# Optimization experiments

Hardware: AMD Instinct MI355X
Metric: run time of the kernel (lower is better)

Reference implementation:

```python
import jax, jax.numpy as jnp
import numpy as np

HIDDEN = 512
HEADS = 8
HEAD_DIM = HIDDEN // HEADS
THRESH = 0.1
EPS = 1e-8


def setup_inputs() -> dict:
    key = jax.random.key(0)
    ks = jax.random.split(key, 9)
    B, S = 2, 4096
    scale = 1.0 / np.sqrt(HIDDEN)
    x = jax.random.normal(ks[0], (B, S, HIDDEN), dtype=jnp.float32)
    Wq = jax.random.normal(ks[1], (HIDDEN, HIDDEN), dtype=jnp.float32) * scale
    bq = jnp.zeros((HIDDEN,), dtype=jnp.float32)
    Wk = jax.random.normal(ks[2], (HIDDEN, HIDDEN), dtype=jnp.float32) * scale
    bk = jnp.zeros((HIDDEN,), dtype=jnp.float32)
    Wv = jax.random.normal(ks[3], (HIDDEN, HIDDEN), dtype=jnp.float32) * scale
    bv = jnp.zeros((HIDDEN,), dtype=jnp.float32)
    Wo = jax.random.normal(ks[4], (HIDDEN, HIDDEN), dtype=jnp.float32) * scale
    bo = jnp.zeros((HIDDEN,), dtype=jnp.float32)
    return {"x": x, "Wq": Wq, "bq": bq, "Wk": Wk, "bk": bk,
            "Wv": Wv, "bv": bv, "Wo": Wo, "bo": bo}


def reference(x, Wq, bq, Wk, bk, Wv, bv, Wo, bo):
    B, S, _ = x.shape
    # torch Linear: y = x @ W.T + b
    def proj(W, b):
        y = jnp.einsum('bsd,ed->bse', x, W) + b
        return y.reshape(B, S, HEADS, HEAD_DIM).transpose(0, 2, 1, 3)  # [B,H,S,Dh]
    Q = proj(Wq, bq)
    K = proj(Wk, bk)
    V = proj(Wv, bv)
    scores = jnp.einsum('bhqd,bhkd->bhqk', Q, K) / jnp.sqrt(jnp.float32(HEAD_DIM))
    probs = jax.nn.softmax(scores, axis=-1)  # [B,H,S,S]
    probs = jnp.where(probs > THRESH, probs, 0.0)
    probs = probs / (jnp.sum(probs, axis=-1, keepdims=True) + EPS)
    ctx = jnp.einsum('bhqk,bhkd->bhqd', probs, V)
    ctx = ctx.transpose(0, 2, 1, 3).reshape(B, S, HIDDEN)
    return jnp.einsum('bsd,ed->bse', ctx, Wo) + bo
```

## Files before the change

kernel.cpp:

```cpp
#include <hip/hip_runtime.h>

#define S_LEN 4096
#define BATCH 2
#define HID 512
#define HEADS 8
#define HD 64
#define NX (BATCH * S_LEN * HID)
#define WSZ (HID * HID)
#define NBH (BATCH * HEADS)
#define QB 64
#define NBLK (S_LEN / QB * NBH)

typedef short v8s __attribute__((ext_vector_type(8)));
typedef float v4f __attribute__((ext_vector_type(4)));
typedef float v16f __attribute__((ext_vector_type(16)));
typedef unsigned short ushort_t;
typedef const __attribute__((address_space(1))) unsigned gu32;
typedef __attribute__((address_space(3))) unsigned lu32;

__device__ __forceinline__ ushort_t f2bf(float f) {
  unsigned u = __builtin_bit_cast(unsigned, f);
  u += 0x7fffu + ((u >> 16) & 1u);
  return (ushort_t)(u >> 16);
}
__device__ __forceinline__ unsigned pk2(float a, float b) {
  return (__builtin_bit_cast(unsigned, a) >> 16) |
         (__builtin_bit_cast(unsigned, b) & 0xFFFF0000u);
}
__device__ __forceinline__ float fexp2(float x) {
  return __builtin_amdgcn_exp2f(x);
}


__global__ __launch_bounds__(256) void cvt_k(
    const float* __restrict__ x,
    const float* __restrict__ wq, const float* __restrict__ wk,
    const float* __restrict__ wv, const float* __restrict__ wo,
    ushort_t* __restrict__ dst)
{
  const size_t e = ((size_t)blockIdx.x * 256 + threadIdx.x) * 4;
  const float* src; size_t off;
  if (e < NX) { src = x; off = e; }
  else {
    const size_t we = e - NX;
    const int wi = (int)(we >> 18);
    src = wi == 0 ? wq : wi == 1 ? wk : wi == 2 ? wv : wo;
    off = we & (WSZ - 1);
  }
  float4 v = *(const float4*)&src[off];
  uint2 u; u.x = pk2(v.x, v.y); u.y = pk2(v.z, v.w);
  *(uint2*)&dst[e] = u;
}

__global__ __launch_bounds__(256) void gemm_qkv(
    const ushort_t* __restrict__ X, const ushort_t* __restrict__ Wb,
    const float* __restrict__ bq, const float* __restrict__ bk, const float* __restrict__ bv,
    ushort_t* __restrict__ Qf, ushort_t* __restrict__ Kf, ushort_t* __restrict__ Vw,
    float qscale)
{
  __shared__ ushort_t As[128][32];
  __shared__ ushort_t Bs[128][32];
  const int t = threadIdx.x;
  const int lane = t & 63;
  const int l15 = lane & 15, lg = lane >> 4;
  const int w = t >> 6;
  const int wr = w >> 1, wc = w & 1;
  const int m0 = blockIdx.y * 128;
  const int wsel = blockIdx.x >> 2;
  const int e0 = (blockIdx.x & 3) * 128;
  const ushort_t* W = Wb + (size_t)wsel * WSZ;
  const float* bias = wsel == 0 ? bq : wsel == 1 ? bk : bv;
  const float osc = (wsel == 0) ? qscale : 1.0f;

  v4f acc[4][4] = {};
  const int r0  = t >> 2;
  const int c0  = (t & 3) * 8;
  const int sc0 = (((t & 3) ^ ((t >> 3) & 3))) * 8;
  const int rsw = (l15 >> 1) & 3;

  for (int k0 = 0; k0 < HID; k0 += 32) {
    __syncthreads();
    __builtin_amdgcn_global_load_lds(
        (gu32*)(const void*)&X[(size_t)(m0 + r0) * HID + k0 + sc0],
        (lu32*)(void*)&As[r0][c0], 16, 0, 0);
    __builtin_amdgcn_global_load_lds(
        (gu32*)(const void*)&X[(size_t)(m0 + r0 + 64) * HID + k0 + sc0],
        (lu32*)(void*)&As[r0 + 64][c0], 16, 0, 0);
    __builtin_amdgcn_global_load_lds(
        (gu32*)(const void*)&W[(size_t)(e0 + r0) * HID + k0 + sc0],
        (lu32*)(void*)&Bs[r0][c0], 16, 0, 0);
    __builtin_amdgcn_global_load_lds(
        (gu32*)(const void*)&W[(size_t)(e0 + r0 + 64) * HID + k0 + sc0],
        (lu32*)(void*)&Bs[r0 + 64][c0], 16, 0, 0);
    __syncthreads();
    v8s a[4], b[4];
    #pragma unroll
    for (int fr = 0; fr < 4; ++fr)
      a[fr] = *(const v8s*)&As[wr * 64 + 16 * fr + l15][8 * (lg ^ rsw)];
    #pragma unroll
    for (int fc = 0; fc < 4; ++fc)
      b[fc] = *(const v8s*)&Bs[wc * 64 + 16 * fc + l15][8 * (lg ^ rsw)];
    #pragma unroll
    for (int fr = 0; fr < 4; ++fr)
      #pragma unroll
      for (int fc = 0; fc < 4; ++fc)
        acc[fr][fc] = __builtin_amdgcn_mfma_f32_16x16x32_bf16(a[fr], b[fc], acc[fr][fc], 0, 0, 0);
  }

  #pragma unroll
  for (int fr = 0; fr < 4; ++fr)
    #pragma unroll
    for (int fc = 0; fc < 4; ++fc) {
      const int e = e0 + wc * 64 + 16 * fc + l15;
      const float bval = bias[e];
      #pragma unroll
      for (int r = 0; r < 4; ++r) {
        const int m = m0 + wr * 64 + 16 * fr + 4 * lg + r;
        const float v = (acc[fr][fc][r] + bval) * osc;
        const int bidx = m >> 12, s = m & (S_LEN - 1);
        const int hh = e >> 6, dh = e & 63;
        const size_t hb = ((size_t)(bidx * HEADS + hh)) * (size_t)(S_LEN * HD);
        if (wsel == 2) {
          Vw[hb + (size_t)s * HD + dh] = f2bf(v);
        } else {
          const size_t off = (size_t)(s >> 5) * 2048 +
              (size_t)(((dh >> 4) * 64 + ((dh >> 3) & 1) * 32 + (s & 31)) * 8 + (dh & 7));
          (wsel == 0 ? Qf : Kf)[hb + off] = f2bf(v);
        }
      }
    }
}

__global__ __launch_bounds__(512, 4) void attn_p1(
    const ushort_t* __restrict__ Qf, const ushort_t* __restrict__ Kf,
    int* __restrict__ Flg)
{
  __shared__ float RedL[4][QB];
  __shared__ float RedM[4][QB];
  __shared__ int bflag;
  const int t = threadIdx.x;
  const int lane = t & 63;
  const int l31 = lane & 31, hi = lane >> 5;
  const int w = t >> 6;
  const int rs = w >> 2;
  const int kq = w & 3;
  const int lin = blockIdx.x;
  const int bh = ((lin & 7) << 1) | ((lin >> 3) & 1);
  const int q0 = (lin >> 4) * QB;
  if (t == 0) bflag = 0;

  const size_t hoff = (size_t)bh * (size_t)(S_LEN * HD);
  const ushort_t* Qb = Qf + hoff + ((size_t)(q0 >> 5) + rs) * 2048;
  const ushort_t* Kb = Kf + hoff;

  v8s qa[4];
  #pragma unroll
  for (int ks = 0; ks < 4; ++ks)
    qa[ks] = *(const v8s*)&Qb[(ks * 64 + lane) * 8];

  float M[16], L[16];
  #pragma unroll
  for (int j = 0; j < 16; ++j) { M[j] = -1e30f; L[j] = 0.f; }

  v8s kA[4], kB[4];

#define LOADK(DST, IDX)                                                     \
  {                                                                         \
    const ushort_t* kc_ = Kb + (size_t)(kq + 4 * (IDX)) * 2048;             \
    _Pragma("unroll")                                                       \
    for (int ks = 0; ks < 4; ++ks)                                          \
      DST[ks] = *(const v8s*)&kc_[(ks * 64 + lane) * 8];                    \
  }
#define CHAIN(KX, OUT)                                                      \
  {                                                                         \
    v16f s_ = {};                                                           \
    _Pragma("unroll")                                                       \
    for (int ks = 0; ks < 4; ++ks)                                          \
      s_ = __builtin_amdgcn_mfma_f32_32x32x16_bf16(qa[ks], KX[ks], s_, 0, 0, 0); \
    OUT = s_;                                                               \
  }
#define MERGE(P)                                                            \
  {                                                                         \
    _Pragma("unroll")                                                       \
    for (int j = 0; j < 16; ++j) {                                          \
      M[j] = fmaxf(M[j], P[j]);                                             \
      L[j] += fexp2(P[j]);                                                  \
    }                                                                       \
  }

  LOADK(kA, 0)
  LOADK(kB, 1)
  v16f prev, cur;
  CHAIN(kA, prev)
  for (int i = 1; i < 31; i += 2) {
    LOADK(kA, i + 1)
    CHAIN(kB, cur)
    MERGE(prev)
    prev = cur;
    LOADK(kB, i + 2)
    CHAIN(kA, cur)
    MERGE(prev)
    prev = cur;
  }
  CHAIN(kB, cur)
  MERGE(prev)
  MERGE(cur)
#undef LOADK
#undef CHAIN
#undef MERGE

  #pragma unroll
  for (int j = 0; j < 16; ++j) {
    float Lv = L[j], Mv = M[j];
    Lv += __shfl_xor(Lv, 1);  Mv = fmaxf(Mv, __shfl_xor(Mv, 1));
    Lv += __shfl_xor(Lv, 2);  Mv = fmaxf(Mv, __shfl_xor(Mv, 2));
    Lv += __shfl_xor(Lv, 4);  Mv = fmaxf(Mv, __shfl_xor(Mv, 4));
    Lv += __shfl_xor(Lv, 8);  Mv = fmaxf(Mv, __shfl_xor(Mv, 8));
    Lv += __shfl_xor(Lv, 16); Mv = fmaxf(Mv, __shfl_xor(Mv, 16));
    if (l31 == 0) {
      const int row = rs * 32 + (j & 3) + 8 * (j >> 2) + 4 * hi;
      RedL[kq][row] = Lv;
      RedM[kq][row] = Mv;
    }
  }
  __syncthreads();
  if (t < QB) {
    const float Lv = RedL[0][t] + RedL[1][t] + RedL[2][t] + RedL[3][t];
    const float Mv = fmaxf(fmaxf(RedM[0][t], RedM[1][t]),
                           fmaxf(RedM[2][t], RedM[3][t]));
    if (Mv >= __log2f(Lv) - 3.3719281f) atomicOr(&bflag, 1);
  }
  __syncthreads();
  if (t == 0) Flg[lin] = bflag;
}

__global__ __launch_bounds__(256) void attn_p2(
    const ushort_t* __restrict__ Qf, const ushort_t* __restrict__ Kf,
    const ushort_t* __restrict__ V, ushort_t* __restrict__ Cb,
    const int* __restrict__ Flg)
{
  const int lin = blockIdx.x;
  if (Flg[lin] == 0) return;
  __shared__ float Osh[QB][HD + 1];
  __shared__ float Dsh[QB];
  __shared__ float RedA[4][QB];
  __shared__ float iLs[QB];
  __shared__ ushort_t Pp[4][32][40];
  __shared__ ushort_t VT[4][HD][40];
  const int t = threadIdx.x;
  const int lane = t & 63;
  const int l31 = lane & 31, hi = lane >> 5;
  const int w = t >> 6;
  const int bh = ((lin & 7) << 1) | ((lin >> 3) & 1);
  const int q0 = (lin >> 4) * QB;
  const size_t hoff = (size_t)bh * (size_t)(S_LEN * HD);
  const ushort_t* Qb = Qf + hoff + (size_t)(q0 >> 5) * 2048;
  const ushort_t* Kb = Kf + hoff;
  const ushort_t* Vh = V + hoff;

  if (t < QB) Dsh[t] = 0.f;
  for (int idx = t; idx < QB * HD; idx += 256) Osh[idx >> 6][idx & 63] = 0.f;

  v8s qa[4], qB[4];
  #pragma unroll
  for (int ks = 0; ks < 4; ++ks) {
    qa[ks] = *(const v8s*)&Qb[(ks * 64 + lane) * 8];
    qB[ks] = *(const v8s*)&Qb[2048 + (ks * 64 + lane) * 8];
  }

  float L0[16], L1[16];
  #pragma unroll
  for (int j = 0; j < 16; ++j) { L0[j] = 0.f; L1[j] = 0.f; }
  for (int i = 0; i < 32; ++i) {
    const ushort_t* kc = Kb + (size_t)(w + 4 * i) * 2048;
    v8s kb[4];
    #pragma unroll
    for (int ks = 0; ks < 4; ++ks)
      kb[ks] = *(const v8s*)&kc[(ks * 64 + lane) * 8];
    v16f sa = {}, sb = {};
    #pragma unroll
    for (int ks = 0; ks < 4; ++ks) {
      sa = __builtin_amdgcn_mfma_f32_32x32x16_bf16(qa[ks], kb[ks], sa, 0, 0, 0);
      sb = __builtin_amdgcn_mfma_f32_32x32x16_bf16(qB[ks], kb[ks], sb, 0, 0, 0);
    }
    #pragma unroll
    for (int j = 0; j < 16; ++j) {
      L0[j] += fexp2(sa[j]);
      L1[j] += fexp2(sb[j]);
    }
  }
  #pragma unroll
  for (int rseti = 0; rseti < 2; ++rseti)
    #pragma unroll
    for (int j = 0; j < 16; ++j) {
      float Lv = (rseti == 0) ? L0[j] : L1[j];
      Lv += __shfl_xor(Lv, 1);  Lv += __shfl_xor(Lv, 2);
      Lv += __shfl_xor(Lv, 4);  Lv += __shfl_xor(Lv, 8);
      Lv += __shfl_xor(Lv, 16);
      if (l31 == 0) {
        const int row = rseti * 32 + (j & 3) + 8 * (j >> 2) + 4 * hi;
        RedA[w][row] = Lv;
      }
    }
  __syncthreads();
  if (t < QB)
    iLs[t] = 1.0f / (RedA[0][t] + RedA[1][t] + RedA[2][t] + RedA[3][t]);
  __syncthreads();

  float il[2][16];
  #pragma unroll
  for (int rseti = 0; rseti < 2; ++rseti)
    #pragma unroll
    for (int j = 0; j < 16; ++j)
      il[rseti][j] = iLs[rseti * 32 + (j & 3) + 8 * (j >> 2) + 4 * hi];

  v16f oA[2] = {}, oB[2] = {};
  float den[2][16] = {};

  for (int i = 0; i < 32; ++i) {
    const int c = w + 4 * i;
    const ushort_t* kc = Kb + (size_t)c * 2048;
    v8s kb[4];
    #pragma unroll
    for (int ks = 0; ks < 4; ++ks)
      kb[ks] = *(const v8s*)&kc[(ks * 64 + lane) * 8];
    v16f sa = {}, sb = {};
    #pragma unroll
    for (int ks = 0; ks < 4; ++ks) {
      sa = __builtin_amdgcn_mfma_f32_32x32x16_bf16(qa[ks], kb[ks], sa, 0, 0, 0);
      sb = __builtin_amdgcn_mfma_f32_32x32x16_bf16(qB[ks], kb[ks], sb, 0, 0, 0);
    }
    {
      const ushort_t* vsrc = &Vh[((size_t)c * 32 + l31) * HD + hi * 32];
      #pragma unroll
      for (int qq = 0; qq < 4; ++qq) {
        uint4 vv = *(const uint4*)&vsrc[qq * 8];
        const ushort_t* pv = (const ushort_t*)&vv;
        #pragma unroll
        for (int jj = 0; jj < 8; ++jj)
          VT[w][hi * 32 + qq * 8 + jj][l31] = pv[jj];
      }
    }
    #pragma unroll
    for (int rseti = 0; rseti < 2; ++rseti) {
      #pragma unroll
      for (int j = 0; j < 16; ++j) {
        const float s = (rseti == 0) ? sa[j] : sb[j];
        const int row = (j & 3) + 8 * (j >> 2) + 4 * hi;
        float p = fexp2(s) * il[rseti][j];
        p = (p > 0.1f) ? p : 0.f;
        den[rseti][j] += p;
        Pp[w][row][l31] = f2bf(p);
      }
      v8s pa0 = *(const v8s*)&Pp[w][l31][8 * hi];
      v8s pa1 = *(const v8s*)&Pp[w][l31][16 + 8 * hi];
      #pragma unroll
      for (int dblk = 0; dblk < 2; ++dblk) {
        v8s vb0 = *(const v8s*)&VT[w][dblk * 32 + l31][8 * hi];
        v8s vb1 = *(const v8s*)&VT[w][dblk * 32 + l31][16 + 8 * hi];
        if (rseti == 0) {
          oA[dblk] = __builtin_amdgcn_mfma_f32_32x32x16_bf16(pa0, vb0, oA[dblk], 0, 0, 0);
          oA[dblk] = __builtin_amdgcn_mfma_f32_32x32x16_bf16(pa1, vb1, oA[dblk], 0, 0, 0);
        } else {
          oB[dblk] = __builtin_amdgcn_mfma_f32_32x32x16_bf16(pa0, vb0, oB[dblk], 0, 0, 0);
          oB[dblk] = __builtin_amdgcn_mfma_f32_32x32x16_bf16(pa1, vb1, oB[dblk], 0, 0, 0);
        }
      }
    }
  }

  #pragma unroll
  for (int rseti = 0; rseti < 2; ++rseti)
    #pragma unroll
    for (int j = 0; j < 16; ++j) {
      float d = den[rseti][j];
      d += __shfl_xor(d, 1); d += __shfl_xor(d, 2); d += __shfl_xor(d, 4);
      d += __shfl_xor(d, 8); d += __shfl_xor(d, 16);
      const int row = rseti * 32 + (j & 3) + 8 * (j >> 2) + 4 * hi;
      if (l31 == 0) atomicAdd(&Dsh[row], d);
    }
  #pragma unroll
  for (int rseti = 0; rseti < 2; ++rseti)
    #pragma unroll
    for (int dblk = 0; dblk < 2; ++dblk)
      #pragma unroll
      for (int j = 0; j < 16; ++j) {
        const int row = rseti * 32 + (j & 3) + 8 * (j >> 2) + 4 * hi;
        const float val = (rseti == 0) ? oA[dblk][j] : oB[dblk][j];
        atomicAdd(&Osh[row][dblk * 32 + l31], val);
      }
  __syncthreads();
  const int b = bh >> 3, h = bh & 7;
  for (int idx = t; idx < QB * HD; idx += 256) {
    const int row = idx >> 6, d = idx & 63;
    const float val = Osh[row][d] / (Dsh[row] + 1e-8f);
    Cb[((size_t)b * S_LEN + q0 + row) * HID + h * HD + d] = f2bf(val);
  }
}

__global__ __launch_bounds__(256) void gemm_out(
    const ushort_t* __restrict__ X, const ushort_t* __restrict__ W,
    const float* __restrict__ bias, const int* __restrict__ Flg,
    float* __restrict__ Df)
{
  const int t = threadIdx.x;
  const int m0 = blockIdx.y * 64;
  const int e0 = blockIdx.x * 64;

  int fm = 0;
  {
    const int b = m0 >> 12, qblk = (m0 & (S_LEN - 1)) >> 6;
    #pragma unroll
    for (int h = 0; h < HEADS; ++h) {
      const int bhh = b * HEADS + h;
      const int base = (bhh >> 1) | ((bhh & 1) << 3);
      fm |= (Flg[base | (qblk << 4)] ? 1 : 0) << h;
    }
    if (!fm) {
      const int row = t >> 2, c0 = (t & 3) * 16;
      #pragma unroll
      for (int g = 0; g < 4; ++g) {
        const float4 bv = *(const float4*)&bias[e0 + c0 + g * 4];
        *(float4*)&Df[(size_t)(m0 + row) * HID + e0 + c0 + g * 4] = bv;
      }
      return;
    }
  }

  __shared__ ushort_t As[64][40];
  __shared__ ushort_t Bs[64][40];
  const int lane = t & 63;
  const int l15 = lane & 15, lg = lane >> 4;
  const int w = t >> 6;
  const int wr = w >> 1, wc = w & 1;

  v4f acc[2][2] = {};
  const int srow = t >> 2, scol = (t & 3) * 8;
  const uint4 zu = {0u, 0u, 0u, 0u};

  for (int k0 = 0; k0 < HID; k0 += 32) {
    __syncthreads();
    const bool hot = (fm >> (k0 >> 6)) & 1;
    *(uint4*)&As[srow][scol] = hot
        ? *(const uint4*)&X[(size_t)(m0 + srow) * HID + k0 + scol]
        : zu;
    *(uint4*)&Bs[srow][scol] =
        *(const uint4*)&W[(size_t)(e0 + srow) * HID + k0 + scol];
    __syncthreads();
    v8s a[2], b[2];
    #pragma unroll
    for (int fr = 0; fr < 2; ++fr)
      a[fr] = *(const v8s*)&As[wr * 32 + 16 * fr + l15][8 * lg];
    #pragma unroll
    for (int fc = 0; fc < 2; ++fc)
      b[fc] = *(const v8s*)&Bs[wc * 32 + 16 * fc + l15][8 * lg];
    #pragma unroll
    for (int fr = 0; fr < 2; ++fr)
      #pragma unroll
      for (int fc = 0; fc < 2; ++fc)
        acc[fr][fc] = __builtin_amdgcn_mfma_f32_16x16x32_bf16(a[fr], b[fc], acc[fr][fc], 0, 0, 0);
  }

  #pragma unroll
  for (int fr = 0; fr < 2; ++fr)
    #pragma unroll
    for (int fc = 0; fc < 2; ++fc) {
      const int e = e0 + wc * 32 + 16 * fc + l15;
      const float bval = bias[e];
      #pragma unroll
      for (int r = 0; r < 4; ++r) {
        const int m = m0 + wr * 32 + 16 * fr + 4 * lg + r;
        Df[(size_t)m * HID + e] = acc[fr][fc][r] + bval;
      }
    }
}

extern "C" void kernel_launch(void* const* d_in, const int* in_sizes, int n_in,
                              void* d_out, int out_size, void* d_ws, size_t ws_size,
                              hipStream_t stream) {
  const float* x  = (const float*)d_in[0];
  const float* Wq = (const float*)d_in[1];
  const float* bq = (const float*)d_in[2];
  const float* Wk = (const float*)d_in[3];
  const float* bk = (const float*)d_in[4];
  const float* Wv = (const float*)d_in[5];
  const float* bv = (const float*)d_in[6];
  const float* Wo = (const float*)d_in[7];
  const float* bo = (const float*)d_in[8];

  int*      Flg  = (int*)d_ws;
  ushort_t* xb   = (ushort_t*)(Flg + NBLK);
  ushort_t* wqb  = xb + NX;
  ushort_t* wob  = wqb + 3 * WSZ;
  ushort_t* Qf   = wob + WSZ;
  ushort_t* Kf   = Qf + NX;
  ushort_t* Vw   = Kf + NX;
  ushort_t* Cb   = Vw + NX;

  const float qscale = 0.125f * 1.44269504f;

  cvt_k<<<(NX + 4 * WSZ) / 1024, 256, 0, stream>>>(x, Wq, Wk, Wv, Wo, xb);

  gemm_qkv<<<dim3(12, 64), 256, 0, stream>>>(
      xb, wqb, bq, bk, bv, Qf, Kf, Vw, qscale);

  attn_p1<<<NBLK, 512, 0, stream>>>(Qf, Kf, Flg);
  attn_p2<<<NBLK, 256, 0, stream>>>(Qf, Kf, Vw, Cb, Flg);

  gemm_out<<<dim3(8, 128), 256, 0, stream>>>(Cb, wob, bo, Flg, (float*)d_out);
}
```

Measured before the change: 103.5 us.

## Switch attention pass-1 scoring to 16x16x32 MFMA with new Q/K fragment layout

Changes the pre-packed Q/K layout from 32-row blocks sized for the 32x32x16 MFMA to 16-row blocks sized for the 16x16x32 bf16 MFMA. Pass 1 (row-max and sum screening) now computes scores as 2x2 tiles of 16x16 products, with smaller accumulators and a shorter shuffle reduction. Pass 2 still uses the 32x32 MFMA, so it now gathers its Q/K fragments element by element through the new layout. Those scalar 2-byte gathers replace the previous 16-byte vector loads and may cost more in pass 2 than pass 1 gains.

```diff
diff --git a/kernel.cpp b/kernel.cpp
--- a/kernel.cpp
+++ b/kernel.cpp
@@ -31,6 +31,10 @@
   return __builtin_amdgcn_exp2f(x);
 }
 
+__device__ __forceinline__ size_t off16(int s, int d) {
+  return (size_t)(s >> 4) * 1024 +
+         (size_t)((d >> 5) * 512 + (((s & 15) + 16 * ((d >> 3) & 3)) * 8) + (d & 7));
+}
 
 __global__ __launch_bounds__(256) void cvt_k(
     const float* __restrict__ x,
@@ -123,9 +127,7 @@
         if (wsel == 2) {
           Vw[hb + (size_t)s * HD + dh] = f2bf(v);
         } else {
-          const size_t off = (size_t)(s >> 5) * 2048 +
-              (size_t)(((dh >> 4) * 64 + ((dh >> 3) & 1) * 32 + (s & 31)) * 8 + (dh & 7));
-          (wsel == 0 ? Qf : Kf)[hb + off] = f2bf(v);
+          (wsel == 0 ? Qf : Kf)[hb + off16(s, dh)] = f2bf(v);
         }
       }
     }
@@ -140,7 +142,7 @@
   __shared__ int bflag;
   const int t = threadIdx.x;
   const int lane = t & 63;
-  const int l31 = lane & 31, hi = lane >> 5;
+  const int l15 = lane & 15, lg = (lane >> 4) & 3;
   const int w = t >> 6;
   const int rs = w >> 2;
   const int kq = w & 3;
@@ -150,57 +152,79 @@
   if (t == 0) bflag = 0;
 
   const size_t hoff = (size_t)bh * (size_t)(S_LEN * HD);
-  const ushort_t* Qb = Qf + hoff + ((size_t)(q0 >> 5) + rs) * 2048;
+  const ushort_t* Qb = Qf + hoff;
   const ushort_t* Kb = Kf + hoff;
 
-  v8s qa[4];
-  #pragma unroll
-  for (int ks = 0; ks < 4; ++ks)
-    qa[ks] = *(const v8s*)&Qb[(ks * 64 + lane) * 8];
-
-  float M[16], L[16];
-  #pragma unroll
-  for (int j = 0; j < 16; ++j) { M[j] = -1e30f; L[j] = 0.f; }
-
-  v8s kA[4], kB[4];
+  v8s qa[2][2];
+  const int qc0 = (q0 >> 4) + rs * 2;
+  #pragma unroll
+  for (int tq = 0; tq < 2; ++tq)
+    #pragma unroll
+    for (int ds = 0; ds < 2; ++ds)
+      qa[tq][ds] = *(const v8s*)&Qb[(size_t)(qc0 + tq) * 1024 + ds * 512 + lane * 8];
+
+  float M[2][4], L[2][4];
+  #pragma unroll
+  for (int tq = 0; tq < 2; ++tq)
+    #pragma unroll
+    for (int r = 0; r < 4; ++r) { M[tq][r] = -1e30f; L[tq][r] = 0.f; }
+
+  v8s kA[2][2], kB[2][2];
 
 #define LOADK(DST, IDX)                                                     \
   {                                                                         \
-    const ushort_t* kc_ = Kb + (size_t)(kq + 4 * (IDX)) * 2048;             \
+    const int kc_ = (kq + 4 * (IDX)) * 2;                                   \
     _Pragma("unroll")                                                       \
-    for (int ks = 0; ks < 4; ++ks)                                          \
-      DST[ks] = *(const v8s*)&kc_[(ks * 64 + lane) * 8];                    \
+    for (int tk = 0; tk < 2; ++tk)                                          \
+      _Pragma("unroll")                                                     \
+      for (int ds = 0; ds < 2; ++ds)                                        \
+        DST[tk][ds] = *(const v8s*)&Kb[(size_t)(kc_ + tk) * 1024 + ds * 512 + lane * 8]; \
   }
 #define CHAIN(KX, OUT)                                                      \
   {                                                                         \
-    v16f s_ = {};                                                           \
     _Pragma("unroll")                                                       \
-    for (int ks = 0; ks < 4; ++ks)                                          \
-      s_ = __builtin_amdgcn_mfma_f32_32x32x16_bf16(qa[ks], KX[ks], s_, 0, 0, 0); \
-    OUT = s_;                                                               \
+    for (int tq = 0; tq < 2; ++tq)                                          \
+      _Pragma("unroll")                                                     \
+      for (int tk = 0; tk < 2; ++tk) {                                      \
+        v4f s_ = {0.f, 0.f, 0.f, 0.f};                                      \
+        s_ = __builtin_amdgcn_mfma_f32_16x16x32_bf16(qa[tq][0], KX[tk][0], s_, 0, 0, 0); \
+        s_ = __builtin_amdgcn_mfma_f32_16x16x32_bf16(qa[tq][1], KX[tk][1], s_, 0, 0, 0); \
+        OUT[tq][tk] = s_;                                                   \
+      }                                                                     \
   }
 #define MERGE(P)                                                            \
   {                                                                         \
     _Pragma("unroll")                                                       \
-    for (int j = 0; j < 16; ++j) {                                          \
-      M[j] = fmaxf(M[j], P[j]);                                             \
-      L[j] += fexp2(P[j]);                                                  \
-    }                                                                       \
+    for (int tq = 0; tq < 2; ++tq)                                          \
+      _Pragma("unroll")                                                     \
+      for (int tk = 0; tk < 2; ++tk)                                        \
+        _Pragma("unroll")                                                   \
+        for (int r = 0; r < 4; ++r) {                                       \
+          M[tq][r] = fmaxf(M[tq][r], P[tq][tk][r]);                         \
+          L[tq][r] += fexp2(P[tq][tk][r]);                                  \
+        }                                                                   \
+  }
+#define CPY(D, S)                                                           \
+  {                                                                         \
+    _Pragma("unroll")                                                       \
+    for (int tq = 0; tq < 2; ++tq)                                          \
+      _Pragma("unroll")                                                     \
+      for (int tk = 0; tk < 2; ++tk) D[tq][tk] = S[tq][tk];                 \
   }
 
   LOADK(kA, 0)
   LOADK(kB, 1)
-  v16f prev, cur;
+  v4f prev[2][2], cur[2][2];
   CHAIN(kA, prev)
   for (int i = 1; i < 31; i += 2) {
     LOADK(kA, i + 1)
     CHAIN(kB, cur)
     MERGE(prev)
-    prev = cur;
+    CPY(prev, cur)
     LOADK(kB, i + 2)
     CHAIN(kA, cur)
     MERGE(prev)
-    prev = cur;
+    CPY(prev, cur)
   }
   CHAIN(kB, cur)
   MERGE(prev)
@@ -208,21 +232,23 @@
 #undef LOADK
 #undef CHAIN
 #undef MERGE
-
-  #pragma unroll
-  for (int j = 0; j < 16; ++j) {
-    float Lv = L[j], Mv = M[j];
-    Lv += __shfl_xor(Lv, 1);  Mv = fmaxf(Mv, __shfl_xor(Mv, 1));
-    Lv += __shfl_xor(Lv, 2);  Mv = fmaxf(Mv, __shfl_xor(Mv, 2));
-    Lv += __shfl_xor(Lv, 4);  Mv = fmaxf(Mv, __shfl_xor(Mv, 4));
-    Lv += __shfl_xor(Lv, 8);  Mv = fmaxf(Mv, __shfl_xor(Mv, 8));
-    Lv += __shfl_xor(Lv, 16); Mv = fmaxf(Mv, __shfl_xor(Mv, 16));
-    if (l31 == 0) {
-      const int row = rs * 32 + (j & 3) + 8 * (j >> 2) + 4 * hi;
-      RedL[kq][row] = Lv;
-      RedM[kq][row] = Mv;
-    }
-  }
+#undef CPY
+
+  #pragma unroll
+  for (int tq = 0; tq < 2; ++tq)
+    #pragma unroll
+    for (int r = 0; r < 4; ++r) {
+      float Lv = L[tq][r], Mv = M[tq][r];
+      Lv += __shfl_xor(Lv, 1);  Mv = fmaxf(Mv, __shfl_xor(Mv, 1));
+      Lv += __shfl_xor(Lv, 2);  Mv = fmaxf(Mv, __shfl_xor(Mv, 2));
+      Lv += __shfl_xor(Lv, 4);  Mv = fmaxf(Mv, __shfl_xor(Mv, 4));
+      Lv += __shfl_xor(Lv, 8);  Mv = fmaxf(Mv, __shfl_xor(Mv, 8));
+      if (l15 == 0) {
+        const int row = rs * 32 + tq * 16 + 4 * lg + r;
+        RedL[kq][row] = Lv;
+        RedM[kq][row] = Mv;
+      }
+    }
   __syncthreads();
   if (t < QB) {
     const float Lv = RedL[0][t] + RedL[1][t] + RedL[2][t] + RedL[3][t];
@@ -254,29 +280,36 @@
   const int bh = ((lin & 7) << 1) | ((lin >> 3) & 1);
   const int q0 = (lin >> 4) * QB;
   const size_t hoff = (size_t)bh * (size_t)(S_LEN * HD);
-  const ushort_t* Qb = Qf + hoff + (size_t)(q0 >> 5) * 2048;
+  const ushort_t* Qb = Qf + hoff;
   const ushort_t* Kb = Kf + hoff;
   const ushort_t* Vh = V + hoff;
 
   if (t < QB) Dsh[t] = 0.f;
   for (int idx = t; idx < QB * HD; idx += 256) Osh[idx >> 6][idx & 63] = 0.f;
 
+#define LD32(DST, BASE, SROW, KS)                                           \
+  { ushort_t tmp_[8];                                                       \
+    _Pragma("unroll")                                                       \
+    for (int j_ = 0; j_ < 8; ++j_)                                          \
+      tmp_[j_] = BASE[off16((SROW), (KS) * 16 + 8 * hi + j_)];              \
+    DST = *(const v8s*)tmp_; }
+
   v8s qa[4], qB[4];
   #pragma unroll
   for (int ks = 0; ks < 4; ++ks) {
-    qa[ks] = *(const v8s*)&Qb[(ks * 64 + lane) * 8];
-    qB[ks] = *(const v8s*)&Qb[2048 + (ks * 64 + lane) * 8];
+    LD32(qa[ks], Qb, q0 + l31, ks)
+    LD32(qB[ks], Qb, q0 + 32 + l31, ks)
   }
 
   float L0[16], L1[16];
   #pragma unroll
   for (int j = 0; j < 16; ++j) { L0[j] = 0.f; L1[j] = 0.f; }
   for (int i = 0; i < 32; ++i) {
-    const ushort_t* kc = Kb + (size_t)(w + 4 * i) * 2048;
+    const int c = w + 4 * i;
     v8s kb[4];
     #pragma unroll
     for (int ks = 0; ks < 4; ++ks)
-      kb[ks] = *(const v8s*)&kc[(ks * 64 + lane) * 8];
+      LD32(kb[ks], Kb, c * 32 + l31, ks)
     v16f sa = {}, sb = {};
     #pragma unroll
     for (int ks = 0; ks < 4; ++ks) {
@@ -319,11 +352,10 @@
 
   for (int i = 0; i < 32; ++i) {
     const int c = w + 4 * i;
-    const ushort_t* kc = Kb + (size_t)c * 2048;
     v8s kb[4];
     #pragma unroll
     for (int ks = 0; ks < 4; ++ks)
-      kb[ks] = *(const v8s*)&kc[(ks * 64 + lane) * 8];
+      LD32(kb[ks], Kb, c * 32 + l31, ks)
     v16f sa = {}, sb = {};
     #pragma unroll
     for (int ks = 0; ks < 4; ++ks) {
@@ -368,6 +400,7 @@
       }
     }
   }
+#undef LD32
 
   #pragma unroll
   for (int rseti = 0; rseti < 2; ++rseti)
```

New measurement: 96.24 us. 7.0% less time.
